# Kernel tuning notes

Hardware: AMD Instinct MI355X
Metric: run time of the kernel (lower is better)

## Reference

```python
import jax, jax.numpy as jnp
import numpy as np

N, E, G, H, L = 50000, 800000, 512, 128, 3
NF, EF = 128, 16
EPS = 1e-5


def _bn(x, g, b):
    # BatchNorm1d in training mode: biased batch statistics over dim 0
    mu = x.mean(0)
    var = x.var(0)
    return g * (x - mu) * jax.lax.rsqrt(var + EPS) + b


def setup_inputs() -> dict:
    key = jax.random.key(0)
    ks = jax.random.split(key, 16)
    s = 0.05
    return {
        "x": jax.random.normal(ks[0], (N, NF), jnp.float32),
        "edge_attr": jax.random.normal(ks[1], (E, EF), jnp.float32),
        "atom_W": jax.random.normal(ks[2], (NF, H), jnp.float32) * s,
        "atom_b": jnp.zeros((H,), jnp.float32),
        "vn_emb": jax.random.normal(ks[3], (H,), jnp.float32) * s,
        "conv_We": jax.random.normal(ks[4], (L, EF, H), jnp.float32) * s,
        "conv_be": jnp.zeros((L, H), jnp.float32),
        "conv_W": jax.random.normal(ks[5], (L, H, H), jnp.float32) * s,
        "conv_b": jnp.zeros((L, H), jnp.float32),
        "conv_g": jnp.ones((L, H), jnp.float32),
        "conv_beta": jnp.zeros((L, H), jnp.float32),
        "vn1_W": jax.random.normal(ks[6], (L, 2 * H, 2 * H), jnp.float32) * s,
        "vn1_b": jnp.zeros((L, 2 * H), jnp.float32),
        "vn1_g": jnp.ones((L, 2 * H), jnp.float32),
        "vn1_beta": jnp.zeros((L, 2 * H), jnp.float32),
        "vn2_W": jax.random.normal(ks[7], (L, 2 * H, H), jnp.float32) * s,
        "vn2_b": jnp.zeros((L, H), jnp.float32),
        "vn2_g": jnp.ones((L, H), jnp.float32),
        "vn2_beta": jnp.zeros((L, H), jnp.float32),
        "pred_W1": jax.random.normal(ks[8], (L * H, L * H), jnp.float32) * s,
        "pred_b1": jnp.zeros((L * H,), jnp.float32),
        "pred_W2": jax.random.normal(ks[9], (L * H, 1), jnp.float32) * s,
        "pred_b2": jnp.zeros((1,), jnp.float32),
        "edge_index": jax.random.randint(ks[10], (2, E), 0, N),
        "batch": jnp.sort(jax.random.randint(ks[11], (N,), 0, G)),
    }


def reference(x, edge_attr, atom_W, atom_b, vn_emb, conv_We, conv_be, conv_W,
              conv_b, conv_g, conv_beta, vn1_W, vn1_b, vn1_g, vn1_beta,
              vn2_W, vn2_b, vn2_g, vn2_beta, pred_W1, pred_b1, pred_W2,
              pred_b2, edge_index, batch):
    src, dst = edge_index[0], edge_index[1]
    h = x @ atom_W + atom_b                      # atom_encoder: [N, H]
    vn = jnp.broadcast_to(vn_emb, (G, H))        # virtual node per graph
    vxs = []
    for i in range(L):
        h = h + vn[batch]                         # gather virtual node by graph id
        # CombConv: edge-conditioned GIN-style message passing
        e = edge_attr @ conv_We[i] + conv_be[i]   # [E, H]
        msg = jax.nn.relu(h[src] + e)             # gather + fuse
        agg = jax.ops.segment_sum(msg, dst, num_segments=N)
        h = jax.nn.relu(_bn((h + agg) @ conv_W[i] + conv_b[i], conv_g[i], conv_beta[i]))
        # virtual node update: gather -> MLP1 -> segment pool -> MLP2
        t = jnp.concatenate([vn[batch], h], axis=-1)          # [N, 2H]
        t = jax.nn.relu(_bn(t @ vn1_W[i] + vn1_b[i], vn1_g[i], vn1_beta[i]))
        pooled = jax.ops.segment_sum(t, batch, num_segments=G)  # global_add_pool
        vn = jax.nn.relu(_bn(pooled @ vn2_W[i] + vn2_b[i], vn2_g[i], vn2_beta[i]))
        vxs.append(vn)
    hg = jnp.concatenate(vxs, axis=-1)            # JK='C': [G, L*H]
    hg = jax.nn.relu(hg @ pred_W1 + pred_b1)
    return hg @ pred_W2 + pred_b2                 # [G, 1]
```

## Files before the change

kernel.cpp:

```cpp
#include <hip/hip_runtime.h>
#include <hip/hip_fp16.h>

constexpr int N = 50000;
constexpr int E = 800000;
constexpr int G = 512;
constexpr int H = 128;
constexpr long long NH = (long long)N * H;
constexpr float EPS = 1e-5f;
constexpr int NB_SCAN = 196;

typedef _Float16 f16x8 __attribute__((ext_vector_type(8)));
typedef _Float16 f16x2 __attribute__((ext_vector_type(2)));
typedef float f32x4 __attribute__((ext_vector_type(4)));

__global__ void k_init_vn(const float* __restrict__ vn_emb, float* __restrict__ vn) {
  int idx = blockIdx.x * 256 + threadIdx.x;
  vn[idx] = vn_emb[idx & 127];
}

__global__ void k_tof16(const float* __restrict__ in, __half* __restrict__ out, int n4) {
  int i = blockIdx.x * 256 + threadIdx.x;
  if (i >= n4) return;
  float4 v = reinterpret_cast<const float4*>(in)[i];
  __half2* o = reinterpret_cast<__half2*>(out);
  o[i * 2]     = __floats2half2_rn(v.x, v.y);
  o[i * 2 + 1] = __floats2half2_rn(v.z, v.w);
}

__global__ void k_wt(const float* __restrict__ W, __half* __restrict__ Wt,
                     int ldw, int row0, int cols, long long wstride, int wtstride) {
  const float* Wl = W + (long long)blockIdx.y * wstride;
  __half* Wtl = Wt + (long long)blockIdx.y * wtstride;
  int idx = blockIdx.x * 256 + threadIdx.x;
  int k = idx & 127, c = idx >> 7;
  Wtl[c * 128 + k] = __float2half(Wl[(long long)(row0 + k) * ldw + c]);
}

__global__ void k_addvn16(__half* __restrict__ h16, const float* __restrict__ vn,
                          const int* __restrict__ batch) {
  int i2 = blockIdx.x * 256 + threadIdx.x;
  int r = i2 >> 6;
  int b = batch[r];
  __half2 hv = reinterpret_cast<__half2*>(h16)[i2];
  float2 vv = reinterpret_cast<const float2*>(vn)[(b << 6) + (i2 & 63)];
  reinterpret_cast<__half2*>(h16)[i2] =
      __floats2half2_rn(__low2float(hv) + vv.x, __high2float(hv) + vv.y);
}

__global__ void k_hist(const int* __restrict__ dst, int* __restrict__ cnt) {
  int e = blockIdx.x * 256 + threadIdx.x;
  atomicAdd(&cnt[dst[e]], 1);
}

__global__ void k_scan_block(const int* __restrict__ cnt, int* __restrict__ off,
                             int* __restrict__ bsum) {
  __shared__ int s[256];
  int idx = blockIdx.x * 256 + threadIdx.x;
  int v = (idx < N) ? cnt[idx] : 0;
  s[threadIdx.x] = v;
  __syncthreads();
  for (int o = 1; o < 256; o <<= 1) {
    int t = (threadIdx.x >= o) ? s[threadIdx.x - o] : 0;
    __syncthreads();
    s[threadIdx.x] += t;
    __syncthreads();
  }
  if (idx < N) off[idx + 1] = s[threadIdx.x];
  if (threadIdx.x == 255) bsum[blockIdx.x] = s[255];
  if (idx == 0) off[0] = 0;
}

__global__ void k_scan_bsum(int* __restrict__ bsum) {
  __shared__ int s[256];
  int v = (threadIdx.x < NB_SCAN) ? bsum[threadIdx.x] : 0;
  s[threadIdx.x] = v;
  __syncthreads();
  for (int o = 1; o < 256; o <<= 1) {
    int t = (threadIdx.x >= o) ? s[threadIdx.x - o] : 0;
    __syncthreads();
    s[threadIdx.x] += t;
    __syncthreads();
  }
  if (threadIdx.x < NB_SCAN) bsum[threadIdx.x] = s[threadIdx.x];
}

__global__ void k_scan_add(int* __restrict__ off, const int* __restrict__ bsum) {
  int idx = blockIdx.x * 256 + threadIdx.x;
  if (idx < N && blockIdx.x > 0) off[idx + 1] += bsum[blockIdx.x - 1];
}

__global__ void k_scatter(const int* __restrict__ src, const int* __restrict__ dst,
                          const int* __restrict__ off, int* __restrict__ cur,
                          int* __restrict__ srcp, __half* __restrict__ eap,
                          const float* __restrict__ edge_attr) {
  int e = blockIdx.x * 256 + threadIdx.x;
  int d = dst[e];
  int p = off[d] + atomicAdd(&cur[d], 1);
  srcp[p] = src[e];
  const float4* ea4 = reinterpret_cast<const float4*>(edge_attr) + e * 4;
  float4 a0 = ea4[0], a1 = ea4[1], a2 = ea4[2], a3 = ea4[3];
  __half2* o = reinterpret_cast<__half2*>(eap + (long long)p * 16);
  o[0] = __floats2half2_rn(a0.x, a0.y);
  o[1] = __floats2half2_rn(a0.z, a0.w);
  o[2] = __floats2half2_rn(a1.x, a1.y);
  o[3] = __floats2half2_rn(a1.z, a1.w);
  o[4] = __floats2half2_rn(a2.x, a2.y);
  o[5] = __floats2half2_rn(a2.z, a2.w);
  o[6] = __floats2half2_rn(a3.x, a3.y);
  o[7] = __floats2half2_rn(a3.z, a3.w);
}

__global__ __launch_bounds__(256) void k_agg(
    const __half* __restrict__ eap, const float* __restrict__ We,
    const float* __restrict__ be, const int* __restrict__ off,
    const int* __restrict__ srcp, const __half* __restrict__ h16,
    __half* __restrict__ hpa16) {
  int tid = threadIdx.x;
  int lane = tid & 63;
  int c0 = lane * 2;
  f16x2 wc0[8], wc1[8];
#pragma unroll
  for (int kk = 0; kk < 8; ++kk) {
    f16x2 w0, w1;
    w0[0] = (_Float16)We[(2 * kk) * 128 + c0];
    w0[1] = (_Float16)We[(2 * kk + 1) * 128 + c0];
    w1[0] = (_Float16)We[(2 * kk) * 128 + c0 + 1];
    w1[1] = (_Float16)We[(2 * kk + 1) * 128 + c0 + 1];
    wc0[kk] = w0; wc1[kk] = w1;
  }
  float2 bev = reinterpret_cast<const float2*>(be)[lane];
  int d = blockIdx.x * 4 + (tid >> 6);
  int j0 = off[d], j1 = off[d + 1];
  const __half2* h2 = reinterpret_cast<const __half2*>(h16);
  const f16x2* e2 = reinterpret_cast<const f16x2*>(eap);
  float a0 = 0.f, a1 = 0.f, b0 = 0.f, b1 = 0.f;
  int j = j0;
  for (; j + 1 < j1; j += 2) {
    int sA = srcp[j], sB = srcp[j + 1];
    __half2 hA = h2[(long long)sA * 64 + lane];
    __half2 hB = h2[(long long)sB * 64 + lane];
    float evA0 = bev.x, evA1 = bev.y, evB0 = bev.x, evB1 = bev.y;
#pragma unroll
    for (int kk = 0; kk < 8; ++kk) {
      f16x2 ea = e2[(long long)j * 8 + kk];
      f16x2 eb = e2[(long long)(j + 1) * 8 + kk];
      evA0 = __builtin_amdgcn_fdot2(ea, wc0[kk], evA0, false);
      evA1 = __builtin_amdgcn_fdot2(ea, wc1[kk], evA1, false);
      evB0 = __builtin_amdgcn_fdot2(eb, wc0[kk], evB0, false);
      evB1 = __builtin_amdgcn_fdot2(eb, wc1[kk], evB1, false);
    }
    a0 += fmaxf(__low2float(hA) + evA0, 0.f);
    a1 += fmaxf(__high2float(hA) + evA1, 0.f);
    b0 += fmaxf(__low2float(hB) + evB0, 0.f);
    b1 += fmaxf(__high2float(hB) + evB1, 0.f);
  }
  if (j < j1) {
    int sA = srcp[j];
    __half2 hA = h2[(long long)sA * 64 + lane];
    float evA0 = bev.x, evA1 = bev.y;
#pragma unroll
    for (int kk = 0; kk < 8; ++kk) {
      f16x2 ea = e2[(long long)j * 8 + kk];
      evA0 = __builtin_amdgcn_fdot2(ea, wc0[kk], evA0, false);
      evA1 = __builtin_amdgcn_fdot2(ea, wc1[kk], evA1, false);
    }
    a0 += fmaxf(__low2float(hA) + evA0, 0.f);
    a1 += fmaxf(__high2float(hA) + evA1, 0.f);
  }
  a0 += b0; a1 += b1;
  __half2 hd = h2[(long long)d * 64 + lane];
  reinterpret_cast<__half2*>(hpa16)[(long long)d * 64 + lane] =
      __floats2half2_rn(__low2float(hd) + a0, __high2float(hd) + a1);
}

template<bool HAS_BIAS, bool HAS_ROWBIAS, bool OUT_F16, bool STATS>
__global__ __launch_bounds__(256) void k_mgemm(
    const __half* __restrict__ A, const __half* __restrict__ Bt,
    const float* __restrict__ bias,
    const float* __restrict__ rowbias, const int* __restrict__ batch,
    float* __restrict__ Cf, __half* __restrict__ Ch,
    float* __restrict__ stats, int ldc, int M) {
  __shared__ _Float16 Ash[64][136];
  __shared__ _Float16 Bsh[128][136];
  int tid = threadIdx.x;
  int m0 = blockIdx.x * 64;
  int c0 = blockIdx.y * 128;
#pragma unroll
  for (int it = 0; it < 4; ++it) {
    int idx = it * 256 + tid;
    int r = idx >> 4, ck = idx & 15;
    f16x8 v = {0, 0, 0, 0, 0, 0, 0, 0};
    if (m0 + r < M)
      v = *reinterpret_cast<const f16x8*>(A + (((long long)(m0 + r)) << 7) + ck * 8);
    *reinterpret_cast<f16x8*>(&Ash[r][ck * 8]) = v;
  }
#pragma unroll
  for (int it = 0; it < 8; ++it) {
    int idx = it * 256 + tid;
    int r = idx >> 4, ck = idx & 15;
    f16x8 v = *reinterpret_cast<const f16x8*>(Bt + (((long long)(c0 + r)) << 7) + ck * 8);
    *reinterpret_cast<f16x8*>(&Bsh[r][ck * 8]) = v;
  }
  __syncthreads();

  int wid = tid >> 6, lane = tid & 63;
  int wr = wid >> 1, wc = wid & 1;
  int lrow = lane & 15;
  int lk = (lane >> 4) * 8;
  f32x4 acc[2][4];
#pragma unroll
  for (int fm = 0; fm < 2; ++fm)
#pragma unroll
    for (int fn = 0; fn < 4; ++fn) acc[fm][fn] = (f32x4){0.f, 0.f, 0.f, 0.f};

#pragma unroll
  for (int kk = 0; kk < 4; ++kk) {
    f16x8 af[2], bf[4];
#pragma unroll
    for (int fm = 0; fm < 2; ++fm)
      af[fm] = *reinterpret_cast<const f16x8*>(&Ash[wr * 32 + fm * 16 + lrow][kk * 32 + lk]);
#pragma unroll
    for (int fn = 0; fn < 4; ++fn)
      bf[fn] = *reinterpret_cast<const f16x8*>(&Bsh[wc * 64 + fn * 16 + lrow][kk * 32 + lk]);
#pragma unroll
    for (int fm = 0; fm < 2; ++fm)
#pragma unroll
      for (int fn = 0; fn < 4; ++fn)
        acc[fm][fn] = __builtin_amdgcn_mfma_f32_16x16x32_f16(af[fm], bf[fn], acc[fm][fn], 0, 0, 0);
  }

  float ss[4], ss2[4];
#pragma unroll
  for (int fn = 0; fn < 4; ++fn) { ss[fn] = 0.f; ss2[fn] = 0.f; }
#pragma unroll
  for (int fn = 0; fn < 4; ++fn) {
    int col = c0 + wc * 64 + fn * 16 + lrow;
    float bb = HAS_BIAS ? bias[col] : 0.f;
#pragma unroll
    for (int fm = 0; fm < 2; ++fm) {
      int grb = m0 + wr * 32 + fm * 16 + (lane >> 4) * 4;
#pragma unroll
      for (int j = 0; j < 4; ++j) {
        int gr = grb + j;
        if (gr < M) {
          float v = acc[fm][fn][j] + bb;
          if (HAS_ROWBIAS)
            v += rowbias[(long long)batch[gr] * ldc + col];
          if (STATS) { ss[fn] += v; ss2[fn] += v * v; }
          if (OUT_F16)
            Ch[(long long)gr * ldc + col] = __float2half(v);
          else
            Cf[(long long)gr * ldc + col] = v;
        }
      }
    }
  }
  if (STATS) {
    __shared__ float sred[2][4][4][16];
#pragma unroll
    for (int fn = 0; fn < 4; ++fn) {
      float s = ss[fn], s2 = ss2[fn];
      s += __shfl_xor(s, 16);  s += __shfl_xor(s, 32);
      s2 += __shfl_xor(s2, 16); s2 += __shfl_xor(s2, 32);
      if (lane < 16) { sred[0][wid][fn][lane] = s; sred[1][wid][fn][lane] = s2; }
    }
    __syncthreads();
    if (wr == 0 && lane < 16) {
#pragma unroll
      for (int fn = 0; fn < 4; ++fn) {
        int col = c0 + wc * 64 + fn * 16 + lane;
        atomicAdd(&stats[col],       sred[0][wid][fn][lane] + sred[0][wid + 2][fn][lane]);
        atomicAdd(&stats[ldc + col], sred[1][wid][fn][lane] + sred[1][wid + 2][fn][lane]);
      }
    }
  }
}

template<int K, bool HAS_BIAS, bool HAS_ROWBIAS, bool RELU>
__global__ __launch_bounds__(256) void k_gemm(
    const float* __restrict__ A1,
    const float* __restrict__ W, int ldw,
    const float* __restrict__ bias,
    const float* __restrict__ rowbias, const int* __restrict__ batch,
    float* __restrict__ C, int M) {
  __shared__ float As[32 * K];
  constexpr int K4 = K / 4;
  int tid = threadIdx.x;
  int m0 = blockIdx.x * 32;
#pragma unroll
  for (int it = 0; it < K / 32; ++it) {
    int e4 = it * 256 + tid;
    int r = e4 / K4;
    int k4 = e4 % K4;
    int gr = m0 + r;
    float4 v = make_float4(0.f, 0.f, 0.f, 0.f);
    if (gr < M) v = reinterpret_cast<const float4*>(A1)[(long long)gr * K4 + k4];
    reinterpret_cast<float4*>(As)[e4] = v;
  }
  __syncthreads();

  int cg = tid & 31;
  int rg = tid >> 5;
  int col = blockIdx.y * 128 + cg * 4;
  float4 acc[4];
#pragma unroll
  for (int j = 0; j < 4; ++j) acc[j] = make_float4(0.f, 0.f, 0.f, 0.f);
  const float4* W4 = reinterpret_cast<const float4*>(W);
  const float4* As4 = reinterpret_cast<const float4*>(As);
#pragma unroll 8
  for (int k = 0; k < K; k += 4) {
    float4 w0 = W4[((k + 0) * ldw + col) >> 2];
    float4 w1 = W4[((k + 1) * ldw + col) >> 2];
    float4 w2 = W4[((k + 2) * ldw + col) >> 2];
    float4 w3 = W4[((k + 3) * ldw + col) >> 2];
#pragma unroll
    for (int j = 0; j < 4; ++j) {
      float4 a = As4[(rg + j * 8) * K4 + (k >> 2)];
      acc[j].x += a.x * w0.x + a.y * w1.x + a.z * w2.x + a.w * w3.x;
      acc[j].y += a.x * w0.y + a.y * w1.y + a.z * w2.y + a.w * w3.y;
      acc[j].z += a.x * w0.z + a.y * w1.z + a.z * w2.z + a.w * w3.z;
      acc[j].w += a.x * w0.w + a.y * w1.w + a.z * w2.w + a.w * w3.w;
    }
  }
  float4 bb = make_float4(0.f, 0.f, 0.f, 0.f);
  if (HAS_BIAS) bb = reinterpret_cast<const float4*>(bias)[blockIdx.y * 32 + cg];
#pragma unroll
  for (int j = 0; j < 4; ++j) {
    int gr = m0 + rg + j * 8;
    if (gr < M) {
      float4 v = acc[j];
      v.x += bb.x; v.y += bb.y; v.z += bb.z; v.w += bb.w;
      if (HAS_ROWBIAS) {
        int b = batch[gr];
        float4 rb = reinterpret_cast<const float4*>(rowbias)[((long long)b * ldw + col) >> 2];
        v.x += rb.x; v.y += rb.y; v.z += rb.z; v.w += rb.w;
      }
      if (RELU) {
        v.x = fmaxf(v.x, 0.f); v.y = fmaxf(v.y, 0.f);
        v.z = fmaxf(v.z, 0.f); v.w = fmaxf(v.w, 0.f);
      }
      reinterpret_cast<float4*>(C)[((long long)gr * ldw + col) >> 2] = v;
    }
  }
}

template<int NC>
__global__ void k_stats(const float* __restrict__ X, int M, float* __restrict__ stats) {
  constexpr int RP = 256 / NC;
  int c = threadIdx.x % NC;
  int rsub = threadIdx.x / NC;
  float s = 0.f, s2 = 0.f;
  for (int r = blockIdx.x * RP + rsub; r < M; r += gridDim.x * RP) {
    float v = X[(long long)r * NC + c];
    s += v; s2 += v * v;
  }
  if (RP > 1) {
    __shared__ float ls[512];
    ls[threadIdx.x] = s; ls[256 + threadIdx.x] = s2;
    __syncthreads();
    if (rsub == 0) {
#pragma unroll
      for (int j = 1; j < RP; ++j) { s += ls[j * NC + c]; s2 += ls[256 + j * NC + c]; }
    }
  }
  if (rsub == 0) { atomicAdd(&stats[c], s); atomicAdd(&stats[NC + c], s2); }
}

__global__ void k_bn16(const float* __restrict__ X, const float* __restrict__ stats,
                       const float* __restrict__ gam, const float* __restrict__ beta,
                       __half* __restrict__ out16, float invM) {
  int i2 = blockIdx.x * 256 + threadIdx.x;
  int c = (i2 & 63) * 2;
  float2 xv = reinterpret_cast<const float2*>(X)[i2];
  float m0 = stats[c] * invM;
  float v0 = stats[128 + c] * invM - m0 * m0;
  float m1 = stats[c + 1] * invM;
  float v1 = stats[128 + c + 1] * invM - m1 * m1;
  float r0 = fmaxf((xv.x - m0) * rsqrtf(v0 + EPS) * gam[c] + beta[c], 0.f);
  float r1 = fmaxf((xv.y - m1) * rsqrtf(v1 + EPS) * gam[c + 1] + beta[c + 1], 0.f);
  reinterpret_cast<__half2*>(out16)[i2] = __floats2half2_rn(r0, r1);
}

__global__ void k_pool(const float* __restrict__ z2, const float* __restrict__ stats,
                       const float* __restrict__ gam, const float* __restrict__ beta,
                       const int* __restrict__ batch, float* __restrict__ pooled) {
  int c = threadIdx.x;
  const float invM = 1.f / (float)N;
  float mean = stats[c] * invM;
  float var = stats[256 + c] * invM - mean * mean;
  float scale = rsqrtf(var + EPS) * gam[c];
  float shift = beta[c] - mean * scale;
  int r0 = blockIdx.x * 128;
  int r1 = min(r0 + 128, N);
  if (r0 >= N) return;
  int curg = batch[r0];
  float acc = 0.f;
  for (int r = r0; r < r1; ++r) {
    int gb = batch[r];
    float v = fmaxf(z2[(long long)r * 256 + c] * scale + shift, 0.f);
    if (gb != curg) { atomicAdd(&pooled[curg * 256 + c], acc); acc = v; curg = gb; }
    else acc += v;
  }
  atomicAdd(&pooled[curg * 256 + c], acc);
}

__global__ void k_vnapply(const float* __restrict__ zvn, const float* __restrict__ stats,
                          const float* __restrict__ gam, const float* __restrict__ beta,
                          float* __restrict__ vn, float* __restrict__ hgbuf, int layer) {
  int idx = blockIdx.x * 256 + threadIdx.x;
  int c = idx & 127;
  int g = idx >> 7;
  const float invM = 1.f / (float)G;
  float mean = stats[c] * invM;
  float var = stats[128 + c] * invM - mean * mean;
  float v = fmaxf((zvn[idx] - mean) * rsqrtf(var + EPS) * gam[c] + beta[c], 0.f);
  vn[idx] = v;
  hgbuf[g * 384 + layer * 128 + c] = v;
}

__global__ void k_pred2(const float* __restrict__ hg2, const float* __restrict__ W2,
                        const float* __restrict__ b2, float* __restrict__ out) {
  int g = blockIdx.x;
  int lane = threadIdx.x;
  float s = 0.f;
  for (int k = lane; k < 384; k += 64) s += hg2[g * 384 + k] * W2[k];
  for (int off = 32; off; off >>= 1) s += __shfl_down(s, off);
  if (lane == 0) out[g] = s + b2[0];
}

extern "C" void kernel_launch(void* const* d_in, const int* in_sizes, int n_in,
                              void* d_out, int out_size, void* d_ws, size_t ws_size,
                              hipStream_t stream) {
  const float* x         = (const float*)d_in[0];
  const float* edge_attr = (const float*)d_in[1];
  const float* atom_W    = (const float*)d_in[2];
  const float* atom_b    = (const float*)d_in[3];
  const float* vn_emb    = (const float*)d_in[4];
  const float* conv_We   = (const float*)d_in[5];
  const float* conv_be   = (const float*)d_in[6];
  const float* conv_W    = (const float*)d_in[7];
  const float* conv_b    = (const float*)d_in[8];
  const float* conv_g    = (const float*)d_in[9];
  const float* conv_beta = (const float*)d_in[10];
  const float* vn1_W     = (const float*)d_in[11];
  const float* vn1_b     = (const float*)d_in[12];
  const float* vn1_g     = (const float*)d_in[13];
  const float* vn1_beta  = (const float*)d_in[14];
  const float* vn2_W     = (const float*)d_in[15];
  const float* vn2_b     = (const float*)d_in[16];
  const float* vn2_g     = (const float*)d_in[17];
  const float* vn2_beta  = (const float*)d_in[18];
  const float* pred_W1   = (const float*)d_in[19];
  const float* pred_b1   = (const float*)d_in[20];
  const float* pred_W2   = (const float*)d_in[21];
  const float* pred_b2   = (const float*)d_in[22];
  const int*   eidx      = (const int*)d_in[23];
  const int*   batch     = (const int*)d_in[24];
  const int* src = eidx;
  const int* dst = eidx + E;

  float* ws    = (float*)d_ws;
  __half* h16  = (__half*)ws;
  float* bufB  = ws + NH / 2;
  __half* hpa16= (__half*)bufB;
  float* z     = bufB + NH;
  float* z2    = bufB;
  __half* x16  = (__half*)z;
  float* U     = bufB + 2 * NH;
  float* pooled= U + G * 256;
  float* zvn   = pooled + G * 256;
  float* vn    = zvn + G * 128;
  float* hgbuf = vn + G * 128;
  float* hg2   = hgbuf + G * 384;
  float* stats = hg2 + G * 384;
  __half* atomWt = (__half*)(stats + 512);
  __half* convWt = atomWt + 16384;
  __half* z2Wt   = convWt + 3 * 16384;
  int*  off    = (int*)(z2Wt + 3 * 32768);
  int*  srcp   = off + 50002;
  __half* eap  = (__half*)(srcp + E);
  int* cnt  = (int*)bufB;
  int* cur  = cnt + N;
  int* bsum = cur + N;

  dim3 b256(256);

  hipMemsetAsync(cnt, 0, (size_t)N * 4, stream);
  hipMemsetAsync(cur, 0, (size_t)N * 4, stream);
  k_hist<<<E / 256, b256, 0, stream>>>(dst, cnt);
  k_scan_block<<<NB_SCAN, b256, 0, stream>>>(cnt, off, bsum);
  k_scan_bsum<<<1, b256, 0, stream>>>(bsum);
  k_scan_add<<<NB_SCAN, b256, 0, stream>>>(off, bsum);
  k_scatter<<<E / 256, b256, 0, stream>>>(src, dst, off, cur, srcp, eap, edge_attr);

  k_init_vn<<<G * 128 / 256, b256, 0, stream>>>(vn_emb, vn);

  k_tof16<<<(N * 128 / 4 + 255) / 256, b256, 0, stream>>>(x, x16, N * 128 / 4);
  k_wt<<<dim3(64, 1), b256, 0, stream>>>(atom_W, atomWt, 128, 0, 128, 0, 0);
  k_wt<<<dim3(64, 3), b256, 0, stream>>>(conv_W, convWt, 128, 0, 128, 16384, 16384);
  k_wt<<<dim3(128, 3), b256, 0, stream>>>(vn1_W, z2Wt, 256, 128, 256, 65536, 32768);

  k_mgemm<true, false, true, false><<<dim3(782, 1), b256, 0, stream>>>(
      x16, atomWt, atom_b, nullptr, nullptr, nullptr, h16, nullptr, 128, N);

  for (int i = 0; i < 3; ++i) {
    k_addvn16<<<12500, b256, 0, stream>>>(h16, vn, batch);
    k_agg<<<12500, b256, 0, stream>>>(eap, conv_We + i * 2048, conv_be + i * 128,
                                      off, srcp, h16, hpa16);
    hipMemsetAsync(stats, 0, 2048, stream);
    k_mgemm<true, false, false, true><<<dim3(782, 1), b256, 0, stream>>>(
        hpa16, convWt + i * 16384, conv_b + i * 128, nullptr, nullptr, z, nullptr,
        stats, 128, N);
    k_bn16<<<12500, b256, 0, stream>>>(z, stats, conv_g + i * 128, conv_beta + i * 128,
                                       h16, 1.f / (float)N);
    k_gemm<128, true, false, false><<<dim3(16, 2), b256, 0, stream>>>(
        vn, vn1_W + i * 256 * 256, 256, vn1_b + i * 256, nullptr, nullptr, U, G);
    hipMemsetAsync(stats, 0, 2048, stream);
    hipMemsetAsync(pooled, 0, (size_t)G * 256 * 4, stream);
    k_mgemm<false, true, false, true><<<dim3(782, 2), b256, 0, stream>>>(
        h16, z2Wt + i * 32768, nullptr, U, batch, z2, nullptr, stats, 256, N);
    k_pool<<<(N + 127) / 128, b256, 0, stream>>>(
        z2, stats, vn1_g + i * 256, vn1_beta + i * 256, batch, pooled);
    k_gemm<256, true, false, false><<<dim3(16, 1), b256, 0, stream>>>(
        pooled, vn2_W + i * 256 * 128, 128, vn2_b + i * 128, nullptr, nullptr, zvn, G);
    hipMemsetAsync(stats, 0, 2048, stream);
    k_stats<128><<<16, b256, 0, stream>>>(zvn, G, stats);
    k_vnapply<<<G * 128 / 256, b256, 0, stream>>>(
        zvn, stats, vn2_g + i * 128, vn2_beta + i * 128, vn, hgbuf, i);
  }
  k_gemm<384, true, false, true><<<dim3(16, 3), b256, 0, stream>>>(
      hgbuf, pred_W1, 384, pred_b1, nullptr, nullptr, hg2, G);
  k_pred2<<<G, 64, 0, stream>>>(hg2, pred_W2, pred_b2, (float*)d_out);
}
```

Baseline: 1.329 ms.

## Store GEMM outputs in fp16, fuse stats, per-graph pooling, wider edge loads

Several independent changes. The conv and vn1 GEMM outputs are now stored in fp16 instead of fp32, which halves the traffic for the BN and pooling passes. The vn2 stats are computed inside the small GEMM, so the separate stats kernel goes away. Pooling now runs one block per graph using precomputed graph start offsets, replacing the atomics. The edge aggregation loop unrolls by 4 with int4 edge-attribute loads, the first vn add is folded into the atom-encoder bias, and the stats memsets are merged into one. Rounding z to fp16 before batch normalization may cost some accuracy.

After: 1.300 ms. 1.02x faster.

```diff
diff --git a/kernel.cpp b/kernel.cpp
--- a/kernel.cpp
+++ b/kernel.cpp
@@ -45,6 +45,14 @@
   float2 vv = reinterpret_cast<const float2*>(vn)[(b << 6) + (i2 & 63)];
   reinterpret_cast<__half2*>(h16)[i2] =
       __floats2half2_rn(__low2float(hv) + vv.x, __high2float(hv) + vv.y);
+}
+
+__global__ void k_gstart(const int* __restrict__ batch, int* __restrict__ gstart) {
+  int g = threadIdx.x;
+  int lo = 0, hi = N;
+  while (lo < hi) { int mid = (lo + hi) >> 1; if (batch[mid] < g) lo = mid + 1; else hi = mid; }
+  gstart[g] = lo;
+  if (g == 0) gstart[G] = N;
 }
 
 __global__ void k_hist(const int* __restrict__ dst, int* __restrict__ cnt) {
@@ -132,42 +140,34 @@
   int d = blockIdx.x * 4 + (tid >> 6);
   int j0 = off[d], j1 = off[d + 1];
   const __half2* h2 = reinterpret_cast<const __half2*>(h16);
-  const f16x2* e2 = reinterpret_cast<const f16x2*>(eap);
+  const int4* e4 = reinterpret_cast<const int4*>(eap);
   float a0 = 0.f, a1 = 0.f, b0 = 0.f, b1 = 0.f;
+  float p0 = 0.f, p1 = 0.f, q0 = 0.f, q1 = 0.f;
   int j = j0;
-  for (; j + 1 < j1; j += 2) {
-    int sA = srcp[j], sB = srcp[j + 1];
-    __half2 hA = h2[(long long)sA * 64 + lane];
-    __half2 hB = h2[(long long)sB * 64 + lane];
-    float evA0 = bev.x, evA1 = bev.y, evB0 = bev.x, evB1 = bev.y;
-#pragma unroll
-    for (int kk = 0; kk < 8; ++kk) {
-      f16x2 ea = e2[(long long)j * 8 + kk];
-      f16x2 eb = e2[(long long)(j + 1) * 8 + kk];
-      evA0 = __builtin_amdgcn_fdot2(ea, wc0[kk], evA0, false);
-      evA1 = __builtin_amdgcn_fdot2(ea, wc1[kk], evA1, false);
-      evB0 = __builtin_amdgcn_fdot2(eb, wc0[kk], evB0, false);
-      evB1 = __builtin_amdgcn_fdot2(eb, wc1[kk], evB1, false);
-    }
-    a0 += fmaxf(__low2float(hA) + evA0, 0.f);
-    a1 += fmaxf(__high2float(hA) + evA1, 0.f);
-    b0 += fmaxf(__low2float(hB) + evB0, 0.f);
-    b1 += fmaxf(__high2float(hB) + evB1, 0.f);
-  }
-  if (j < j1) {
-    int sA = srcp[j];
-    __half2 hA = h2[(long long)sA * 64 + lane];
-    float evA0 = bev.x, evA1 = bev.y;
-#pragma unroll
-    for (int kk = 0; kk < 8; ++kk) {
-      f16x2 ea = e2[(long long)j * 8 + kk];
-      evA0 = __builtin_amdgcn_fdot2(ea, wc0[kk], evA0, false);
-      evA1 = __builtin_amdgcn_fdot2(ea, wc1[kk], evA1, false);
-    }
-    a0 += fmaxf(__low2float(hA) + evA0, 0.f);
-    a1 += fmaxf(__high2float(hA) + evA1, 0.f);
-  }
-  a0 += b0; a1 += b1;
+#define EDGE(J, A0, A1) do {                                                   \
+    int s_ = srcp[(J)];                                                        \
+    __half2 hv_ = h2[(long long)s_ * 64 + lane];                               \
+    int4 lo_ = e4[2 * (J)], hi_ = e4[2 * (J) + 1];                             \
+    float ev0_ = bev.x, ev1_ = bev.y;                                          \
+    int w_[8] = {lo_.x, lo_.y, lo_.z, lo_.w, hi_.x, hi_.y, hi_.z, hi_.w};      \
+    _Pragma("unroll")                                                          \
+    for (int kk = 0; kk < 8; ++kk) {                                           \
+      f16x2 ea_ = __builtin_bit_cast(f16x2, w_[kk]);                           \
+      ev0_ = __builtin_amdgcn_fdot2(ea_, wc0[kk], ev0_, false);                \
+      ev1_ = __builtin_amdgcn_fdot2(ea_, wc1[kk], ev1_, false);                \
+    }                                                                          \
+    A0 += fmaxf(__low2float(hv_) + ev0_, 0.f);                                 \
+    A1 += fmaxf(__high2float(hv_) + ev1_, 0.f);                                \
+  } while (0)
+  for (; j + 3 < j1; j += 4) {
+    EDGE(j, a0, a1);
+    EDGE(j + 1, b0, b1);
+    EDGE(j + 2, p0, p1);
+    EDGE(j + 3, q0, q1);
+  }
+  for (; j < j1; ++j) EDGE(j, a0, a1);
+#undef EDGE
+  a0 += b0 + p0 + q0; a1 += b1 + p1 + q1;
   __half2 hd = h2[(long long)d * 64 + lane];
   reinterpret_cast<__half2*>(hpa16)[(long long)d * 64 + lane] =
       __floats2half2_rn(__low2float(hd) + a0, __high2float(hd) + a1);
@@ -176,7 +176,7 @@
 template<bool HAS_BIAS, bool HAS_ROWBIAS, bool OUT_F16, bool STATS>
 __global__ __launch_bounds__(256) void k_mgemm(
     const __half* __restrict__ A, const __half* __restrict__ Bt,
-    const float* __restrict__ bias,
+    const float* __restrict__ bias, const float* __restrict__ bias2,
     const float* __restrict__ rowbias, const int* __restrict__ batch,
     float* __restrict__ Cf, __half* __restrict__ Ch,
     float* __restrict__ stats, int ldc, int M) {
@@ -236,6 +236,7 @@
   for (int fn = 0; fn < 4; ++fn) {
     int col = c0 + wc * 64 + fn * 16 + lrow;
     float bb = HAS_BIAS ? bias[col] : 0.f;
+    if (HAS_BIAS && bias2 != nullptr) bb += bias2[col];
 #pragma unroll
     for (int fm = 0; fm < 2; ++fm) {
       int grb = m0 + wr * 32 + fm * 16 + (lane >> 4) * 4;
@@ -276,13 +277,13 @@
   }
 }
 
-template<int K, bool HAS_BIAS, bool HAS_ROWBIAS, bool RELU>
+template<int K, bool HAS_BIAS, bool HAS_ROWBIAS, bool RELU, bool STATS>
 __global__ __launch_bounds__(256) void k_gemm(
     const float* __restrict__ A1,
     const float* __restrict__ W, int ldw,
     const float* __restrict__ bias,
     const float* __restrict__ rowbias, const int* __restrict__ batch,
-    float* __restrict__ C, int M) {
+    float* __restrict__ C, float* __restrict__ stats, int M) {
   __shared__ float As[32 * K];
   constexpr int K4 = K / 4;
   int tid = threadIdx.x;
@@ -297,6 +298,8 @@
     if (gr < M) v = reinterpret_cast<const float4*>(A1)[(long long)gr * K4 + k4];
     reinterpret_cast<float4*>(As)[e4] = v;
   }
+  __shared__ float cs[128], cs2[128];
+  if (STATS && tid < 128) { cs[tid] = 0.f; cs2[tid] = 0.f; }
   __syncthreads();
 
   int cg = tid & 31;
@@ -324,6 +327,7 @@
   }
   float4 bb = make_float4(0.f, 0.f, 0.f, 0.f);
   if (HAS_BIAS) bb = reinterpret_cast<const float4*>(bias)[blockIdx.y * 32 + cg];
+  float ps[4] = {0.f, 0.f, 0.f, 0.f}, ps2[4] = {0.f, 0.f, 0.f, 0.f};
 #pragma unroll
   for (int j = 0; j < 4; ++j) {
     int gr = m0 + rg + j * 8;
@@ -339,69 +343,61 @@
         v.x = fmaxf(v.x, 0.f); v.y = fmaxf(v.y, 0.f);
         v.z = fmaxf(v.z, 0.f); v.w = fmaxf(v.w, 0.f);
       }
+      if (STATS) {
+        ps[0] += v.x; ps2[0] += v.x * v.x;
+        ps[1] += v.y; ps2[1] += v.y * v.y;
+        ps[2] += v.z; ps2[2] += v.z * v.z;
+        ps[3] += v.w; ps2[3] += v.w * v.w;
+      }
       reinterpret_cast<float4*>(C)[((long long)gr * ldw + col) >> 2] = v;
     }
   }
-}
-
-template<int NC>
-__global__ void k_stats(const float* __restrict__ X, int M, float* __restrict__ stats) {
-  constexpr int RP = 256 / NC;
-  int c = threadIdx.x % NC;
-  int rsub = threadIdx.x / NC;
-  float s = 0.f, s2 = 0.f;
-  for (int r = blockIdx.x * RP + rsub; r < M; r += gridDim.x * RP) {
-    float v = X[(long long)r * NC + c];
-    s += v; s2 += v * v;
-  }
-  if (RP > 1) {
-    __shared__ float ls[512];
-    ls[threadIdx.x] = s; ls[256 + threadIdx.x] = s2;
+  if (STATS) {
+#pragma unroll
+    for (int jc = 0; jc < 4; ++jc) {
+      atomicAdd(&cs[cg * 4 + jc], ps[jc]);
+      atomicAdd(&cs2[cg * 4 + jc], ps2[jc]);
+    }
     __syncthreads();
-    if (rsub == 0) {
-#pragma unroll
-      for (int j = 1; j < RP; ++j) { s += ls[j * NC + c]; s2 += ls[256 + j * NC + c]; }
-    }
-  }
-  if (rsub == 0) { atomicAdd(&stats[c], s); atomicAdd(&stats[NC + c], s2); }
-}
-
-__global__ void k_bn16(const float* __restrict__ X, const float* __restrict__ stats,
+    if (tid < 128) {
+      atomicAdd(&stats[blockIdx.y * 128 + tid], cs[tid]);
+      atomicAdd(&stats[ldw + blockIdx.y * 128 + tid], cs2[tid]);
+    }
+  }
+}
+
+__global__ void k_bn16(const __half* __restrict__ X16, const float* __restrict__ stats,
                        const float* __restrict__ gam, const float* __restrict__ beta,
                        __half* __restrict__ out16, float invM) {
   int i2 = blockIdx.x * 256 + threadIdx.x;
   int c = (i2 & 63) * 2;
-  float2 xv = reinterpret_cast<const float2*>(X)[i2];
+  __half2 xv = reinterpret_cast<const __half2*>(X16)[i2];
   float m0 = stats[c] * invM;
   float v0 = stats[128 + c] * invM - m0 * m0;
   float m1 = stats[c + 1] * invM;
   float v1 = stats[128 + c + 1] * invM - m1 * m1;
-  float r0 = fmaxf((xv.x - m0) * rsqrtf(v0 + EPS) * gam[c] + beta[c], 0.f);
-  float r1 = fmaxf((xv.y - m1) * rsqrtf(v1 + EPS) * gam[c + 1] + beta[c + 1], 0.f);
+  float r0 = fmaxf((__low2float(xv) - m0) * rsqrtf(v0 + EPS) * gam[c] + beta[c], 0.f);
+  float r1 = fmaxf((__high2float(xv) - m1) * rsqrtf(v1 + EPS) * gam[c + 1] + beta[c + 1], 0.f);
   reinterpret_cast<__half2*>(out16)[i2] = __floats2half2_rn(r0, r1);
 }
 
-__global__ void k_pool(const float* __restrict__ z2, const float* __restrict__ stats,
+__global__ void k_pool(const __half* __restrict__ z2_16, const float* __restrict__ stats,
                        const float* __restrict__ gam, const float* __restrict__ beta,
-                       const int* __restrict__ batch, float* __restrict__ pooled) {
-  int c = threadIdx.x;
+                       const int* __restrict__ gstart, float* __restrict__ pooled) {
+  int g = blockIdx.x;
+  int c = blockIdx.y * 128 + threadIdx.x;
   const float invM = 1.f / (float)N;
   float mean = stats[c] * invM;
   float var = stats[256 + c] * invM - mean * mean;
   float scale = rsqrtf(var + EPS) * gam[c];
   float shift = beta[c] - mean * scale;
-  int r0 = blockIdx.x * 128;
-  int r1 = min(r0 + 128, N);
-  if (r0 >= N) return;
-  int curg = batch[r0];
+  int r0 = gstart[g], r1 = gstart[g + 1];
   float acc = 0.f;
   for (int r = r0; r < r1; ++r) {
-    int gb = batch[r];
-    float v = fmaxf(z2[(long long)r * 256 + c] * scale + shift, 0.f);
-    if (gb != curg) { atomicAdd(&pooled[curg * 256 + c], acc); acc = v; curg = gb; }
-    else acc += v;
-  }
-  atomicAdd(&pooled[curg * 256 + c], acc);
+    float v = __half2float(z2_16[(long long)r * 256 + c]);
+    acc += fmaxf(v * scale + shift, 0.f);
+  }
+  pooled[g * 256 + c] = acc;
 }
 
 __global__ void k_vnapply(const float* __restrict__ zvn, const float* __restrict__ stats,
@@ -463,17 +459,19 @@
   __half* h16  = (__half*)ws;
   float* bufB  = ws + NH / 2;
   __half* hpa16= (__half*)bufB;
-  float* z     = bufB + NH;
-  float* z2    = bufB;
-  __half* x16  = (__half*)z;
-  float* U     = bufB + 2 * NH;
+  __half* z16  = (__half*)(bufB + NH / 2);
+  __half* x16  = z16;
+  __half* z2_16= (__half*)(bufB + NH);
+  float* smallz= bufB + 2 * NH;
+  float* U     = smallz;
   float* pooled= U + G * 256;
   float* zvn   = pooled + G * 256;
   float* vn    = zvn + G * 128;
   float* hgbuf = vn + G * 128;
   float* hg2   = hgbuf + G * 384;
-  float* stats = hg2 + G * 384;
-  __half* atomWt = (__half*)(stats + 512);
+  float* statsz= hg2 + G * 384;
+  int*   gstart= (int*)(statsz + 3 * 1024);
+  __half* atomWt = (__half*)(gstart + 516);
   __half* convWt = atomWt + 16384;
   __half* z2Wt   = convWt + 3 * 16384;
   int*  off    = (int*)(z2Wt + 3 * 32768);
@@ -487,11 +485,13 @@
 
   hipMemsetAsync(cnt, 0, (size_t)N * 4, stream);
   hipMemsetAsync(cur, 0, (size_t)N * 4, stream);
+  hipMemsetAsync(statsz, 0, 3 * 1024 * 4, stream);
   k_hist<<<E / 256, b256, 0, stream>>>(dst, cnt);
   k_scan_block<<<NB_SCAN, b256, 0, stream>>>(cnt, off, bsum);
   k_scan_bsum<<<1, b256, 0, stream>>>(bsum);
   k_scan_add<<<NB_SCAN, b256, 0, stream>>>(off, bsum);
   k_scatter<<<E / 256, b256, 0, stream>>>(src, dst, off, cur, srcp, eap, edge_attr);
+  k_gstart<<<1, G, 0, stream>>>(batch, gstart);
 
   k_init_vn<<<G * 128 / 256, b256, 0, stream>>>(vn_emb, vn);
 
@@ -501,34 +501,32 @@
   k_wt<<<dim3(128, 3), b256, 0, stream>>>(vn1_W, z2Wt, 256, 128, 256, 65536, 32768);
 
   k_mgemm<true, false, true, false><<<dim3(782, 1), b256, 0, stream>>>(
-      x16, atomWt, atom_b, nullptr, nullptr, nullptr, h16, nullptr, 128, N);
+      x16, atomWt, atom_b, vn_emb, nullptr, nullptr, nullptr, h16, nullptr, 128, N);
 
   for (int i = 0; i < 3; ++i) {
-    k_addvn16<<<12500, b256, 0, stream>>>(h16, vn, batch);
+    float* SZ = statsz + i * 1024;
+    if (i > 0) k_addvn16<<<12500, b256, 0, stream>>>(h16, vn, batch);
     k_agg<<<12500, b256, 0, stream>>>(eap, conv_We + i * 2048, conv_be + i * 128,
                                       off, srcp, h16, hpa16);
-    hipMemsetAsync(stats, 0, 2048, stream);
-    k_mgemm<true, false, false, true><<<dim3(782, 1), b256, 0, stream>>>(
-        hpa16, convWt + i * 16384, conv_b + i * 128, nullptr, nullptr, z, nullptr,
-        stats, 128, N);
-    k_bn16<<<12500, b256, 0, stream>>>(z, stats, conv_g + i * 128, conv_beta + i * 128,
+    k_mgemm<true, false, true, true><<<dim3(782, 1), b256, 0, stream>>>(
+        hpa16, convWt + i * 16384, conv_b + i * 128, nullptr, nullptr, nullptr,
+        nullptr, z16, SZ, 128, N);
+    k_bn16<<<12500, b256, 0, stream>>>(z16, SZ, conv_g + i * 128, conv_beta + i * 128,
                                        h16, 1.f / (float)N);
-    k_gemm<128, true, false, false><<<dim3(16, 2), b256, 0, stream>>>(
-        vn, vn1_W + i * 256 * 256, 256, vn1_b + i * 256, nullptr, nullptr, U, G);
-    hipMemsetAsync(stats, 0, 2048, stream);
-    hipMemsetAsync(pooled, 0, (size_t)G * 256 * 4, stream);
-    k_mgemm<false, true, false, true><<<dim3(782, 2), b256, 0, stream>>>(
-        h16, z2Wt + i * 32768, nullptr, U, batch, z2, nullptr, stats, 256, N);
-    k_pool<<<(N + 127) / 128, b256, 0, stream>>>(
-        z2, stats, vn1_g + i * 256, vn1_beta + i * 256, batch, pooled);
-    k_gemm<256, true, false, false><<<dim3(16, 1), b256, 0, stream>>>(
-        pooled, vn2_W + i * 256 * 128, 128, vn2_b + i * 128, nullptr, nullptr, zvn, G);
-    hipMemsetAsync(stats, 0, 2048, stream);
-    k_stats<128><<<16, b256, 0, stream>>>(zvn, G, stats);
+    k_gemm<128, true, false, false, false><<<dim3(16, 2), b256, 0, stream>>>(
+        vn, vn1_W + i * 256 * 256, 256, vn1_b + i * 256, nullptr, nullptr, U, nullptr, G);
+    k_mgemm<false, true, true, true><<<dim3(782, 2), b256, 0, stream>>>(
+        h16, z2Wt + i * 32768, nullptr, nullptr, U, batch, nullptr, z2_16,
+        SZ + 256, 256, N);
+    k_pool<<<dim3(G, 2), dim3(128), 0, stream>>>(
+        z2_16, SZ + 256, vn1_g + i * 256, vn1_beta + i * 256, gstart, pooled);
+    k_gemm<256, true, false, false, true><<<dim3(16, 1), b256, 0, stream>>>(
+        pooled, vn2_W + i * 256 * 128, 128, vn2_b + i * 128, nullptr, nullptr,
+        zvn, SZ + 768, G);
     k_vnapply<<<G * 128 / 256, b256, 0, stream>>>(
-        zvn, stats, vn2_g + i * 128, vn2_beta + i * 128, vn, hgbuf, i);
-  }
-  k_gemm<384, true, false, true><<<dim3(16, 3), b256, 0, stream>>>(
-      hgbuf, pred_W1, 384, pred_b1, nullptr, nullptr, hg2, G);
+        zvn, SZ + 768, vn2_g + i * 128, vn2_beta + i * 128, vn, hgbuf, i);
+  }
+  k_gemm<384, true, false, true, false><<<dim3(16, 3), b256, 0, stream>>>(
+      hgbuf, pred_W1, 384, pred_b1, nullptr, nullptr, hg2, nullptr, G);
   k_pred2<<<G, 64, 0, stream>>>(hg2, pred_W2, pred_b2, (float*)d_out);
 }
```
